# Performance work log

Measured on AMD Instinct MI355X. Metric: run time of the kernel, lower is better.

Reference implementation:

```python
import jax, jax.numpy as jnp
import numpy as np
import math

B, S, H = 2, 2048, 3072
NH, NKV, HD = 32, 32, 96
BASE = 10000.0
NEG = -1e9


def rotate_half(x):
    x1 = x[..., : x.shape[-1] // 2]
    x2 = x[..., x.shape[-1] // 2 :]
    return jnp.concatenate((-x2, x1), axis=-1)


def setup_inputs() -> dict:
    key = jax.random.key(0)
    k1, k2, k3 = jax.random.split(key, 3)
    hidden_states = jax.random.normal(k1, (B, S, H), dtype=jnp.float32)
    position_ids = jnp.broadcast_to(jnp.arange(S, dtype=jnp.int32), (B, S))
    # additive causal mask: 0 where key <= query, -1e9 above the diagonal
    i = jnp.arange(S)
    causal = jnp.where(i[None, :] <= i[:, None], 0.0, NEG).astype(jnp.float32)
    attention_mask = jnp.broadcast_to(causal[None, None], (B, 1, S, S))
    w_qkv = jax.random.normal(k2, (NH * HD + 2 * NKV * HD, H), dtype=jnp.float32) * 0.02
    w_o = jax.random.normal(k3, (H, NH * HD), dtype=jnp.float32) * 0.02
    return {
        "hidden_states": hidden_states,
        "position_ids": position_ids,
        "attention_mask": attention_mask,
        "w_qkv": w_qkv,
        "w_o": w_o,
    }


def reference(hidden_states, position_ids, attention_mask, w_qkv, w_o):
    bsz, q_len, _ = hidden_states.shape
    # fused QKV projection (no bias), then split per Phi3 layout
    qkv = jnp.einsum("bsh,oh->bso", hidden_states, w_qkv)
    q = qkv[..., : NH * HD]
    k = qkv[..., NH * HD : NH * HD + NKV * HD]
    v = qkv[..., NH * HD + NKV * HD :]
    q = q.reshape(bsz, q_len, NH, HD).transpose(0, 2, 1, 3)   # [B,NH,S,HD]
    k = k.reshape(bsz, q_len, NKV, HD).transpose(0, 2, 1, 3)  # [B,NKV,S,HD]
    v = v.reshape(bsz, q_len, NKV, HD).transpose(0, 2, 1, 3)

    # rotary embeddings (Phi3RotaryEmbedding, no scaling)
    inv_freq = 1.0 / (BASE ** (jnp.arange(0, HD, 2, dtype=jnp.float32) / HD))  # [HD/2]
    freqs = position_ids.astype(jnp.float32)[:, :, None] * inv_freq[None, None, :]  # [B,S,HD/2]
    emb = jnp.concatenate((freqs, freqs), axis=-1)  # [B,S,HD]
    cos = jnp.cos(emb)[:, None].astype(hidden_states.dtype)  # [B,1,S,HD]
    sin = jnp.sin(emb)[:, None].astype(hidden_states.dtype)
    q = q * cos + rotate_half(q) * sin
    k = k * cos + rotate_half(k) * sin
    # num_key_value_groups = NH // NKV = 1 -> repeat_kv is a no-op

    attn = jnp.einsum("bhqd,bhkd->bhqk", q, k) / math.sqrt(HD)
    attn = attn + attention_mask  # broadcast over heads
    attn = jax.nn.softmax(attn.astype(jnp.float32), axis=-1).astype(v.dtype)
    # attention_dropout = 0.0 / eval mode -> dropout is identity
    out = jnp.einsum("bhqk,bhkd->bhqd", attn, v)
    out = out.transpose(0, 2, 1, 3).reshape(bsz, q_len, NH * HD)
    return jnp.einsum("bso,ho->bsh", out, w_o)
```

## Files before the change

### kernel.cpp

```cpp
#include <hip/hip_runtime.h>
#include <hip/hip_bf16.h>
#include <type_traits>

typedef unsigned short ushort_t;
typedef __attribute__((ext_vector_type(8))) short bf16x8;
typedef __attribute__((ext_vector_type(4))) float f32x4;

#define S_LEN 2048
#define NHEAD 32
#define HDIM 96

__device__ __forceinline__ float bf2f(ushort_t b) {
    union { unsigned u; float f; } v; v.u = ((unsigned)b) << 16; return v.f;
}
__device__ __forceinline__ ushort_t f2bf(float f) {
    union { float f; unsigned u; } v; v.f = f;
    unsigned r = v.u + 0x7fffu + ((v.u >> 16) & 1u);
    return (ushort_t)(r >> 16);
}
__device__ __forceinline__ void cp16(ushort_t* l, const ushort_t* g) {
    __builtin_amdgcn_global_load_lds((const __attribute__((address_space(1))) void*)g,
                                     (__attribute__((address_space(3))) void*)l, 16, 0, 0);
}

__global__ void cvt_f32_bf16(const float* __restrict__ src, ushort_t* __restrict__ dst, int n8)
{
    const int i = blockIdx.x * 256 + threadIdx.x;
    if (i >= n8) return;
    const float4 a = ((const float4*)src)[2 * i];
    const float4 b = ((const float4*)src)[2 * i + 1];
    union { ushort_t us[8]; int4 v; } r;
    r.us[0] = f2bf(a.x); r.us[1] = f2bf(a.y); r.us[2] = f2bf(a.z); r.us[3] = f2bf(a.w);
    r.us[4] = f2bf(b.x); r.us[5] = f2bf(b.y); r.us[6] = f2bf(b.z); r.us[7] = f2bf(b.w);
    ((int4*)dst)[i] = r.v;
}

__global__ __launch_bounds__(768, 3) void gemm288(
    const ushort_t* __restrict__ A, const ushort_t* __restrict__ Bm,
    ushort_t* __restrict__ C, int M, int N, int K)
{
    __shared__ ushort_t As[2][16384];
    __shared__ ushort_t Bs[2][18432];
    const int tid = threadIdx.x;
    const int lane = tid & 63, w = tid >> 6;
    const int wm = w / 6, wn = w % 6;
    const int r16 = lane & 15, quad = lane >> 4;

    const int m0 = blockIdx.y * 256;
    const int n0 = blockIdx.x * 288;

    const ushort_t* gp[3];
    ushort_t* lp[3];
    int bstr[3], pstr[3];
#pragma unroll
    for (int j = 0; j < 3; j++) {
        int c = tid + 768 * j;
        if (c >= 2176) c -= 2176;
        if (c < 1024) {
            const int row = c >> 2;
            gp[j] = A + (size_t)(m0 + row) * K + (((c & 3) ^ ((row >> 1) & 3)) * 8);
            lp[j] = &As[0][c * 8];
            bstr[j] = 16384; pstr[j] = 8192;
        } else {
            const int cb = c - 1024;
            const int row = cb >> 2;
            gp[j] = Bm + (size_t)(n0 + row) * K + (((cb & 3) ^ ((row >> 1) & 3)) * 8);
            lp[j] = &Bs[0][cb * 8];
            bstr[j] = 18432; pstr[j] = 9216;
        }
    }
#define STAGE(buf, ks, ko) { \
    cp16(lp[0] + (buf) * bstr[0] + (ks) * pstr[0], gp[0] + (ko) + (ks) * 32); \
    cp16(lp[1] + (buf) * bstr[1] + (ks) * pstr[1], gp[1] + (ko) + (ks) * 32); \
    cp16(lp[2] + (buf) * bstr[2] + (ks) * pstr[2], gp[2] + (ko) + (ks) * 32); }

    const int laneoff = r16 * 32 + (quad ^ ((r16 >> 1) & 3)) * 8;

    f32x4 acc[8][3];
#pragma unroll
    for (int m = 0; m < 8; m++)
#pragma unroll
        for (int j = 0; j < 3; j++) acc[m][j] = f32x4{0.f, 0.f, 0.f, 0.f};

    const int NT = K >> 6;

    STAGE(0, 0, 0);
    STAGE(0, 1, 0);
    asm volatile("s_waitcnt vmcnt(0)" ::: "memory");
    __builtin_amdgcn_s_barrier();
    asm volatile("" ::: "memory");

    for (int t = 0; t < NT; ++t) {
        const int b = t & 1, bn = b ^ 1;
        const int ko = (t + 1) << 6;
        bf16x8 av[8], bv[3];

#pragma unroll
        for (int j = 0; j < 3; j++)
            bv[j] = *(const bf16x8*)&Bs[b][(wn * 48 + j * 16) * 32 + laneoff];
#pragma unroll
        for (int m = 0; m < 8; m++)
            av[m] = *(const bf16x8*)&As[b][(wm * 128 + m * 16) * 32 + laneoff];
        if (t + 1 < NT) { STAGE(bn, 0, ko); STAGE(bn, 1, ko); }
        __builtin_amdgcn_s_setprio(1);
#pragma unroll
        for (int m = 0; m < 8; m++)
#pragma unroll
            for (int j = 0; j < 3; j++)
                acc[m][j] = __builtin_amdgcn_mfma_f32_16x16x32_bf16(av[m], bv[j], acc[m][j], 0, 0, 0);
        __builtin_amdgcn_s_setprio(0);
#pragma unroll
        for (int j = 0; j < 3; j++)
            bv[j] = *(const bf16x8*)&Bs[b][9216 + (wn * 48 + j * 16) * 32 + laneoff];
#pragma unroll
        for (int m = 0; m < 8; m++)
            av[m] = *(const bf16x8*)&As[b][8192 + (wm * 128 + m * 16) * 32 + laneoff];
        __builtin_amdgcn_s_setprio(1);
#pragma unroll
        for (int m = 0; m < 8; m++)
#pragma unroll
            for (int j = 0; j < 3; j++)
                acc[m][j] = __builtin_amdgcn_mfma_f32_16x16x32_bf16(av[m], bv[j], acc[m][j], 0, 0, 0);
        __builtin_amdgcn_s_setprio(0);
        asm volatile("s_waitcnt vmcnt(0)" ::: "memory");
        __builtin_amdgcn_s_barrier();
        asm volatile("" ::: "memory");
    }
#undef STAGE

#pragma unroll
    for (int m = 0; m < 8; m++) {
        const int row0 = m0 + wm * 128 + m * 16 + quad * 4;
#pragma unroll
        for (int j = 0; j < 3; j++) {
            const int col = n0 + wn * 48 + j * 16 + r16;
#pragma unroll
            for (int r = 0; r < 4; r++)
                C[(size_t)(row0 + r) * N + col] = f2bf(acc[m][j][r]);
        }
    }
}

template <typename OT>
__global__ __launch_bounds__(512, 2) void gemm256(
    const ushort_t* __restrict__ A, const ushort_t* __restrict__ Bm,
    OT* __restrict__ C, int M, int N, int K)
{
    __shared__ ushort_t As[2][16384];
    __shared__ ushort_t Bs[2][12288];
    const int tid = threadIdx.x;
    const int lane = tid & 63, w = tid >> 6;
    const int wm = w >> 2, wn = w & 3;
    const int r16 = lane & 15, quad = lane >> 4;

    const int m0 = blockIdx.y * 256;
    const int n0 = blockIdx.x * 192;

    const int sl8 = ((tid & 3) ^ ((tid >> 3) & 3)) * 8;
    const int srow = tid >> 2;
    const ushort_t* gA  = A  + (size_t)(m0 + srow) * K + sl8;
    const size_t rsk = (size_t)128 * K;
    const ushort_t* gB0 = Bm + (size_t)(n0 + srow) * K + sl8;
    const ushort_t* gB1 = Bm + (size_t)(n0 + ((tid < 256) ? (128 + srow) : ((tid - 256) >> 2))) * K
                          + ((tid < 256) ? 0 : 32) + sl8;
    const ushort_t* gB2 = Bm + (size_t)(n0 + 64 + srow) * K + 32 + sl8;

    const int laneoff = r16 * 32 + (quad ^ ((r16 >> 1) & 3)) * 8;

    f32x4 acc[8][3];
#pragma unroll
    for (int m = 0; m < 8; m++)
#pragma unroll
        for (int j = 0; j < 3; j++) acc[m][j] = f32x4{0.f, 0.f, 0.f, 0.f};

    const int NT = K >> 6;

#define STAGE_ALL(bn, kb) { \
    cp16(&Bs[bn][tid * 8],         gB0 + (kb)); \
    cp16(&Bs[bn][tid * 8 + 4096],  gB1 + (kb)); \
    cp16(&Bs[bn][tid * 8 + 8192],  gB2 + (kb)); \
    cp16(&As[bn][tid * 8],         gA + (kb)); \
    cp16(&As[bn][tid * 8 + 4096],  gA + rsk + (kb)); \
    cp16(&As[bn][tid * 8 + 8192],  gA + (kb) + 32); \
    cp16(&As[bn][tid * 8 + 12288], gA + rsk + (kb) + 32); }

    STAGE_ALL(0, 0);
    asm volatile("s_waitcnt vmcnt(0)" ::: "memory");
    __builtin_amdgcn_s_barrier();
    asm volatile("" ::: "memory");

    for (int t = 0; t < NT; ++t) {
        const int b = t & 1, bn = b ^ 1;
        const int kb = (t + 1) << 6;
        bf16x8 av[8], bv[3];

#pragma unroll
        for (int j = 0; j < 3; j++)
            bv[j] = *(const bf16x8*)&Bs[b][(wn * 48 + j * 16) * 32 + laneoff];
#pragma unroll
        for (int m = 0; m < 8; m++)
            av[m] = *(const bf16x8*)&As[b][(wm * 128 + m * 16) * 32 + laneoff];
        if (t + 1 < NT) STAGE_ALL(bn, kb);
        __builtin_amdgcn_s_setprio(1);
#pragma unroll
        for (int m = 0; m < 8; m++)
#pragma unroll
            for (int j = 0; j < 3; j++)
                acc[m][j] = __builtin_amdgcn_mfma_f32_16x16x32_bf16(av[m], bv[j], acc[m][j], 0, 0, 0);
        __builtin_amdgcn_s_setprio(0);
#pragma unroll
        for (int j = 0; j < 3; j++)
            bv[j] = *(const bf16x8*)&Bs[b][6144 + (wn * 48 + j * 16) * 32 + laneoff];
#pragma unroll
        for (int m = 0; m < 8; m++)
            av[m] = *(const bf16x8*)&As[b][8192 + (wm * 128 + m * 16) * 32 + laneoff];
        __builtin_amdgcn_s_setprio(1);
#pragma unroll
        for (int m = 0; m < 8; m++)
#pragma unroll
            for (int j = 0; j < 3; j++)
                acc[m][j] = __builtin_amdgcn_mfma_f32_16x16x32_bf16(av[m], bv[j], acc[m][j], 0, 0, 0);
        __builtin_amdgcn_s_setprio(0);
        asm volatile("s_waitcnt vmcnt(0)" ::: "memory");
        __builtin_amdgcn_s_barrier();
        asm volatile("" ::: "memory");
    }
#undef STAGE_ALL

#pragma unroll
    for (int m = 0; m < 8; m++) {
        const int row0 = m0 + wm * 128 + m * 16 + quad * 4;
#pragma unroll
        for (int j = 0; j < 3; j++) {
            const int col = n0 + wn * 48 + j * 16 + r16;
#pragma unroll
            for (int r = 0; r < 4; r++) {
                if constexpr (std::is_same<OT, float>::value)
                    C[(size_t)(row0 + r) * N + col] = acc[m][j][r];
                else
                    C[(size_t)(row0 + r) * N + col] = f2bf(acc[m][j][r]);
            }
        }
    }
}

__global__ void rope_scatter(const ushort_t* __restrict__ qkv, const int* __restrict__ pos,
                             ushort_t* __restrict__ Q, ushort_t* __restrict__ Kd)
{
    const int d = threadIdx.x;
    const int t = blockIdx.x * 2 + threadIdx.y;
    const int h = blockIdx.y;
    const int which = d >= 48;
    const int dd = which ? d - 48 : d;
    const int p = pos[t];
    const float inv = exp2f((float)dd * (-13.287712379549449f / 48.0f));
    const float th = (float)p * inv;
    const float cs = cosf(th), sn = sinf(th);
    const ushort_t* src = qkv + (size_t)t * 9216 + (which ? 3072 : 0) + h * 96;
    const float x1 = bf2f(src[dd]), x2 = bf2f(src[dd + 48]);
    ushort_t* dst = (which ? Kd : Q) +
        ((size_t)((t >> 11) * NHEAD + h) * S_LEN + (t & 2047)) * HDIM;
    dst[dd]      = f2bf(x1 * cs - x2 * sn);
    dst[dd + 48] = f2bf(x2 * cs + x1 * sn);
}

__global__ __launch_bounds__(256) void v_transpose2(const ushort_t* __restrict__ qkv,
                                                    ushort_t* __restrict__ VT)
{
    __shared__ ushort_t tl[64 * 102];
    const int tid = threadIdx.x;
    const int s0 = blockIdx.x * 64;
    const int h  = blockIdx.y;
    const int b  = blockIdx.z;
    const ushort_t* src = qkv + ((size_t)(b * 2048 + s0)) * 9216 + 6144 + h * 96;
#pragma unroll
    for (int k = 0; k < 24; k++) {
        const int idx = tid + 256 * k;
        const int r = idx / 96, c = idx % 96;
        tl[r * 102 + c] = src[(size_t)r * 9216 + c];
    }
    __syncthreads();
    ushort_t* dst = VT + (size_t)(b * NHEAD + h) * HDIM * S_LEN + s0;
#pragma unroll
    for (int k = 0; k < 24; k++) {
        const int idx = tid + 256 * k;
        const int d = idx >> 6, s = idx & 63;
        dst[(size_t)d * S_LEN + s] = tl[s * 102 + d];
    }
}

__global__ __launch_bounds__(256, 2) void flash_attn(
    const ushort_t* __restrict__ Q, const ushort_t* __restrict__ Kg,
    const ushort_t* __restrict__ VT, ushort_t* __restrict__ attn)
{
    __shared__ ushort_t Qs[128 * 104];
    __shared__ ushort_t Ps[128 * 72];

    const int tid = threadIdx.x, w = tid >> 6, lane = tid & 63;
    const int r16 = lane & 15, quad = lane >> 4;
    const int qi = 15 - (blockIdx.x >> 6);
    const int bh = blockIdx.x & 63;
    const int q0 = qi * 128;
    const ushort_t* Qg  = Q  + ((size_t)bh * S_LEN + q0) * HDIM;
    const ushort_t* Kgb = Kg + (size_t)bh * S_LEN * HDIM;
    const ushort_t* Vgb = VT + (size_t)bh * HDIM * S_LEN;

#pragma unroll
    for (int c = 0; c < 6; c++) {
        const int cc = tid + 256 * c;
        const int row = cc / 12, col = (cc % 12) * 8;
        *(int4*)&Qs[row * 104 + col] = *(const int4*)(Qg + row * 96 + col);
    }
    __syncthreads();

    float m_st[2][4], l_st[2][4];
#pragma unroll
    for (int i = 0; i < 2; i++)
#pragma unroll
        for (int r = 0; r < 4; r++) { m_st[i][r] = -1.0e30f; l_st[i][r] = 0.f; }

    f32x4 o[2][6];
#pragma unroll
    for (int i = 0; i < 2; i++)
#pragma unroll
        for (int jo = 0; jo < 6; jo++) o[i][jo] = f32x4{0.f, 0.f, 0.f, 0.f};

    const float sc = 0.10206207261596577f;
    const float L2E = 1.4426950408889634f;
    const int nkt = 2 * qi + 2;
    const int rowb = 32 * w;

    for (int kt = 0; kt < nkt; ++kt) {
        const int k0 = kt * 64;

        f32x4 sacc[2][4];
#pragma unroll
        for (int i = 0; i < 2; i++)
#pragma unroll
            for (int j = 0; j < 4; j++) sacc[i][j] = f32x4{0.f, 0.f, 0.f, 0.f};
#pragma unroll
        for (int kk = 0; kk < 3; kk++) {
            bf16x8 qa[2], kb[4];
#pragma unroll
            for (int i = 0; i < 2; i++)
                qa[i] = *(const bf16x8*)&Qs[(rowb + 16 * i + r16) * 104 + kk * 32 + quad * 8];
#pragma unroll
            for (int j = 0; j < 4; j++)
                kb[j] = *(const bf16x8*)(Kgb + (size_t)(k0 + 16 * j + r16) * 96
                                         + kk * 32 + quad * 8);
            __builtin_amdgcn_s_setprio(1);
#pragma unroll
            for (int i = 0; i < 2; i++)
#pragma unroll
                for (int j = 0; j < 4; j++)
                    sacc[i][j] = __builtin_amdgcn_mfma_f32_16x16x32_bf16(qa[i], kb[j], sacc[i][j], 0, 0, 0);
            __builtin_amdgcn_s_setprio(0);
        }

        const bool need_mask = (kt >= 2 * qi);
#pragma unroll
        for (int i = 0; i < 2; i++)
#pragma unroll
            for (int j = 0; j < 4; j++)
#pragma unroll
                for (int r = 0; r < 4; r++) {
                    float v = sacc[i][j][r] * sc;
                    if (need_mask) {
                        const int grow = q0 + rowb + 16 * i + quad * 4 + r;
                        const int gcol = k0 + 16 * j + r16;
                        if (gcol > grow) v = -1.0e9f;
                    }
                    sacc[i][j][r] = v;
                }

        float mt[2][4];
#pragma unroll
        for (int i = 0; i < 2; i++)
#pragma unroll
            for (int r = 0; r < 4; r++) {
                float mp = fmaxf(fmaxf(sacc[i][0][r], sacc[i][1][r]),
                                 fmaxf(sacc[i][2][r], sacc[i][3][r]));
                mp = fmaxf(mp, __shfl_xor(mp, 1, 16));
                mp = fmaxf(mp, __shfl_xor(mp, 2, 16));
                mp = fmaxf(mp, __shfl_xor(mp, 4, 16));
                mp = fmaxf(mp, __shfl_xor(mp, 8, 16));
                mt[i][r] = mp;
            }

        float alpha[2][4];
#pragma unroll
        for (int i = 0; i < 2; i++)
#pragma unroll
            for (int r = 0; r < 4; r++) {
                const float mn = fmaxf(m_st[i][r], mt[i][r]);
                alpha[i][r] = exp2f((m_st[i][r] - mn) * L2E);
                m_st[i][r] = mn;
            }

        float psum[2][4];
#pragma unroll
        for (int i = 0; i < 2; i++)
#pragma unroll
            for (int r = 0; r < 4; r++) psum[i][r] = 0.f;
#pragma unroll
        for (int i = 0; i < 2; i++)
#pragma unroll
            for (int j = 0; j < 4; j++)
#pragma unroll
                for (int r = 0; r < 4; r++) {
                    const float p = exp2f((sacc[i][j][r] - m_st[i][r]) * L2E);
                    psum[i][r] += p;
                    Ps[(rowb + 16 * i + quad * 4 + r) * 72 + 16 * j + r16] = f2bf(p);
                }
#pragma unroll
        for (int i = 0; i < 2; i++)
#pragma unroll
            for (int r = 0; r < 4; r++) {
                float s2 = psum[i][r];
                s2 += __shfl_xor(s2, 1, 16);
                s2 += __shfl_xor(s2, 2, 16);
                s2 += __shfl_xor(s2, 4, 16);
                s2 += __shfl_xor(s2, 8, 16);
                l_st[i][r] = l_st[i][r] * alpha[i][r] + s2;
            }

#pragma unroll
        for (int i = 0; i < 2; i++)
#pragma unroll
            for (int jo = 0; jo < 6; jo++)
#pragma unroll
                for (int r = 0; r < 4; r++) o[i][jo][r] *= alpha[i][r];
#pragma unroll
        for (int kk = 0; kk < 2; kk++) {
            bf16x8 pa[2], vb[6];
#pragma unroll
            for (int i = 0; i < 2; i++)
                pa[i] = *(const bf16x8*)&Ps[(rowb + 16 * i + r16) * 72 + kk * 32 + quad * 8];
#pragma unroll
            for (int jo = 0; jo < 6; jo++)
                vb[jo] = *(const bf16x8*)(Vgb + (size_t)(16 * jo + r16) * S_LEN
                                          + k0 + kk * 32 + quad * 8);
            __builtin_amdgcn_s_setprio(1);
#pragma unroll
            for (int i = 0; i < 2; i++)
#pragma unroll
                for (int jo = 0; jo < 6; jo++)
                    o[i][jo] = __builtin_amdgcn_mfma_f32_16x16x32_bf16(pa[i], vb[jo], o[i][jo], 0, 0, 0);
            __builtin_amdgcn_s_setprio(0);
        }
    }

    const int b = bh >> 5, h = bh & 31;
#pragma unroll
    for (int i = 0; i < 2; i++)
#pragma unroll
        for (int r = 0; r < 4; r++) {
            const int lr = rowb + 16 * i + quad * 4 + r;
            const float inv = 1.0f / l_st[i][r];
            const size_t base = (size_t)(b * S_LEN + q0 + lr) * 3072 + h * 96;
#pragma unroll
            for (int jo = 0; jo < 6; jo++)
                attn[base + 16 * jo + r16] = f2bf(o[i][jo][r] * inv);
        }
}

extern "C" void kernel_launch(void* const* d_in, const int* in_sizes, int n_in,
                              void* d_out, int out_size, void* d_ws, size_t ws_size,
                              hipStream_t stream)
{
    const float* hidden = (const float*)d_in[0];
    const int*   pos    = (const int*)d_in[1];
    const float* w_qkv  = (const float*)d_in[3];
    const float* w_o    = (const float*)d_in[4];
    float* out          = (float*)d_out;

    char* ws = (char*)d_ws;
    ushort_t* hbf    = (ushort_t*)(ws);
    ushort_t* wqkvbf = (ushort_t*)(ws + 25165824);
    ushort_t* Qb     = (ushort_t*)(ws);
    ushort_t* Kb     = (ushort_t*)(ws + 25165824);
    ushort_t* VTb    = (ushort_t*)(ws + 50331648);
    ushort_t* qkv    = (ushort_t*)(ws + 81788928);
    ushort_t* attn   = qkv;
    ushort_t* wobf   = (ushort_t*)(ws + 157286400);

    cvt_f32_bf16<<<dim3(12582912 / 8 / 256), 256, 0, stream>>>(hidden, hbf, 12582912 / 8);
    cvt_f32_bf16<<<dim3(28311552 / 8 / 256), 256, 0, stream>>>(w_qkv, wqkvbf, 28311552 / 8);
    cvt_f32_bf16<<<dim3(9437184 / 8 / 256), 256, 0, stream>>>(w_o, wobf, 9437184 / 8);

    gemm288<<<dim3(32, 16), 768, 0, stream>>>(hbf, wqkvbf, qkv, 4096, 9216, 3072);
    rope_scatter<<<dim3(2048, 32), dim3(96, 2), 0, stream>>>(qkv, pos, Qb, Kb);
    v_transpose2<<<dim3(32, 32, 2), 256, 0, stream>>>(qkv, VTb);
    flash_attn<<<dim3(1024), 256, 0, stream>>>(Qb, Kb, VTb, attn);
    gemm256<float><<<dim3(16, 16), 512, 0, stream>>>(attn, wobf, out, 4096, 3072, 3072);
}
```

Baseline: 764.5 us.

## Add lazy softmax rescaling, Q in registers, balanced tile order, higher occupancy

Q fragments now stay in registers instead of being staged through shared memory, and launch bounds rise to 4 blocks per SM. The q-tile order is interleaved so long and short causal tiles mix across the grid. The score scale and log2e are folded into one FMA constant. The online-softmax rescale of O and l is skipped unless the row max grows past a threshold anywhere in the wave. It also drops setprio hints and uses a near -inf mask value, at the cost of more register pressure under the higher occupancy target.

Result: slower. 865.1 us (+13.2%).

```diff
diff --git a/kernel.cpp b/kernel.cpp
--- a/kernel.cpp
+++ b/kernel.cpp
@@ -289,29 +289,31 @@
     }
 }
 
-__global__ __launch_bounds__(256, 2) void flash_attn(
+__global__ __launch_bounds__(256, 4) void flash_attn(
     const ushort_t* __restrict__ Q, const ushort_t* __restrict__ Kg,
     const ushort_t* __restrict__ VT, ushort_t* __restrict__ attn)
 {
-    __shared__ ushort_t Qs[128 * 104];
     __shared__ ushort_t Ps[128 * 72];
 
     const int tid = threadIdx.x, w = tid >> 6, lane = tid & 63;
     const int r16 = lane & 15, quad = lane >> 4;
-    const int qi = 15 - (blockIdx.x >> 6);
+    static const int qmap[16] = {15,13,11,9, 8,10,12,14, 7,5,3,1, 0,2,4,6};
+    const int qi = qmap[blockIdx.x >> 6];
     const int bh = blockIdx.x & 63;
     const int q0 = qi * 128;
     const ushort_t* Qg  = Q  + ((size_t)bh * S_LEN + q0) * HDIM;
     const ushort_t* Kgb = Kg + (size_t)bh * S_LEN * HDIM;
     const ushort_t* Vgb = VT + (size_t)bh * HDIM * S_LEN;
 
-#pragma unroll
-    for (int c = 0; c < 6; c++) {
-        const int cc = tid + 256 * c;
-        const int row = cc / 12, col = (cc % 12) * 8;
-        *(int4*)&Qs[row * 104 + col] = *(const int4*)(Qg + row * 96 + col);
-    }
-    __syncthreads();
+    const int rowb = 32 * w;
+
+    bf16x8 qreg[3][2];
+#pragma unroll
+    for (int kk = 0; kk < 3; kk++)
+#pragma unroll
+        for (int i = 0; i < 2; i++)
+            qreg[kk][i] = *(const bf16x8*)(Qg + (size_t)(rowb + 16 * i + r16) * 96
+                                           + kk * 32 + quad * 8);
 
     float m_st[2][4], l_st[2][4];
 #pragma unroll
@@ -325,10 +327,9 @@
 #pragma unroll
         for (int jo = 0; jo < 6; jo++) o[i][jo] = f32x4{0.f, 0.f, 0.f, 0.f};
 
-    const float sc = 0.10206207261596577f;
-    const float L2E = 1.4426950408889634f;
+    const float CS  = 0.14724920020342437f;
+    const float RTH = 54.329f;
     const int nkt = 2 * qi + 2;
-    const int rowb = 32 * w;
 
     for (int kt = 0; kt < nkt; ++kt) {
         const int k0 = kt * 64;
@@ -340,38 +341,30 @@
             for (int j = 0; j < 4; j++) sacc[i][j] = f32x4{0.f, 0.f, 0.f, 0.f};
 #pragma unroll
         for (int kk = 0; kk < 3; kk++) {
-            bf16x8 qa[2], kb[4];
-#pragma unroll
-            for (int i = 0; i < 2; i++)
-                qa[i] = *(const bf16x8*)&Qs[(rowb + 16 * i + r16) * 104 + kk * 32 + quad * 8];
+            bf16x8 kb[4];
 #pragma unroll
             for (int j = 0; j < 4; j++)
                 kb[j] = *(const bf16x8*)(Kgb + (size_t)(k0 + 16 * j + r16) * 96
                                          + kk * 32 + quad * 8);
-            __builtin_amdgcn_s_setprio(1);
 #pragma unroll
             for (int i = 0; i < 2; i++)
 #pragma unroll
                 for (int j = 0; j < 4; j++)
-                    sacc[i][j] = __builtin_amdgcn_mfma_f32_16x16x32_bf16(qa[i], kb[j], sacc[i][j], 0, 0, 0);
-            __builtin_amdgcn_s_setprio(0);
-        }
-
-        const bool need_mask = (kt >= 2 * qi);
-#pragma unroll
-        for (int i = 0; i < 2; i++)
-#pragma unroll
-            for (int j = 0; j < 4; j++)
-#pragma unroll
-                for (int r = 0; r < 4; r++) {
-                    float v = sacc[i][j][r] * sc;
-                    if (need_mask) {
+                    sacc[i][j] = __builtin_amdgcn_mfma_f32_16x16x32_bf16(qreg[kk][i], kb[j], sacc[i][j], 0, 0, 0);
+        }
+
+        if (kt >= 2 * qi) {
+#pragma unroll
+            for (int i = 0; i < 2; i++)
+#pragma unroll
+                for (int j = 0; j < 4; j++)
+#pragma unroll
+                    for (int r = 0; r < 4; r++) {
                         const int grow = q0 + rowb + 16 * i + quad * 4 + r;
                         const int gcol = k0 + 16 * j + r16;
-                        if (gcol > grow) v = -1.0e9f;
+                        if (gcol > grow) sacc[i][j][r] = -3.0e38f;
                     }
-                    sacc[i][j][r] = v;
-                }
+        }
 
         float mt[2][4];
 #pragma unroll
@@ -387,16 +380,36 @@
                 mt[i][r] = mp;
             }
 
-        float alpha[2][4];
-#pragma unroll
-        for (int i = 0; i < 2; i++)
-#pragma unroll
-            for (int r = 0; r < 4; r++) {
-                const float mn = fmaxf(m_st[i][r], mt[i][r]);
-                alpha[i][r] = exp2f((m_st[i][r] - mn) * L2E);
-                m_st[i][r] = mn;
-            }
-
+        int okl = 1;
+#pragma unroll
+        for (int i = 0; i < 2; i++)
+#pragma unroll
+            for (int r = 0; r < 4; r++)
+                okl &= (mt[i][r] - m_st[i][r] <= RTH) ? 1 : 0;
+        if (!__all(okl)) {
+            float alpha[2][4];
+#pragma unroll
+            for (int i = 0; i < 2; i++)
+#pragma unroll
+                for (int r = 0; r < 4; r++) {
+                    const float mn = fmaxf(m_st[i][r], mt[i][r]);
+                    alpha[i][r] = exp2f((m_st[i][r] - mn) * CS);
+                    m_st[i][r] = mn;
+                    l_st[i][r] *= alpha[i][r];
+                }
+#pragma unroll
+            for (int i = 0; i < 2; i++)
+#pragma unroll
+                for (int jo = 0; jo < 6; jo++)
+#pragma unroll
+                    for (int r = 0; r < 4; r++) o[i][jo][r] *= alpha[i][r];
+        }
+
+        float nmcs[2][4];
+#pragma unroll
+        for (int i = 0; i < 2; i++)
+#pragma unroll
+            for (int r = 0; r < 4; r++) nmcs[i][r] = -m_st[i][r] * CS;
         float psum[2][4];
 #pragma unroll
         for (int i = 0; i < 2; i++)
@@ -408,7 +421,7 @@
             for (int j = 0; j < 4; j++)
 #pragma unroll
                 for (int r = 0; r < 4; r++) {
-                    const float p = exp2f((sacc[i][j][r] - m_st[i][r]) * L2E);
+                    const float p = exp2f(fmaf(sacc[i][j][r], CS, nmcs[i][r]));
                     psum[i][r] += p;
                     Ps[(rowb + 16 * i + quad * 4 + r) * 72 + 16 * j + r16] = f2bf(p);
                 }
@@ -421,15 +434,9 @@
                 s2 += __shfl_xor(s2, 2, 16);
                 s2 += __shfl_xor(s2, 4, 16);
                 s2 += __shfl_xor(s2, 8, 16);
-                l_st[i][r] = l_st[i][r] * alpha[i][r] + s2;
+                l_st[i][r] += s2;
             }
 
-#pragma unroll
-        for (int i = 0; i < 2; i++)
-#pragma unroll
-            for (int jo = 0; jo < 6; jo++)
-#pragma unroll
-                for (int r = 0; r < 4; r++) o[i][jo][r] *= alpha[i][r];
 #pragma unroll
         for (int kk = 0; kk < 2; kk++) {
             bf16x8 pa[2], vb[6];
@@ -440,13 +447,11 @@
             for (int jo = 0; jo < 6; jo++)
                 vb[jo] = *(const bf16x8*)(Vgb + (size_t)(16 * jo + r16) * S_LEN
                                           + k0 + kk * 32 + quad * 8);
-            __builtin_amdgcn_s_setprio(1);
 #pragma unroll
             for (int i = 0; i < 2; i++)
 #pragma unroll
                 for (int jo = 0; jo < 6; jo++)
                     o[i][jo] = __builtin_amdgcn_mfma_f32_16x16x32_bf16(pa[i], vb[jo], o[i][jo], 0, 0, 0);
-            __builtin_amdgcn_s_setprio(0);
         }
     }
 
```
